# Kernel tuning notes

Hardware: AMD Instinct MI355X
Metric: run time of the kernel (lower is better)

The kernel has to match this reference:

```python
import jax, jax.numpy as jnp
import numpy as np
from jax import lax

# NPZD biogeochemistry constants (fixed buffers in the torch module)
XI = 0.067; ZETA = 0.0095; LAM = 0.06; PSI = 1.46; MU = 0.25; ETA = 1.5; KAP = 1.0
DT = 0.125        # time step in days (trange[1]-trange[0])
SPD = 8           # steps per day = round(1/DT)


def weno3z(qm, q0, qp):
    eps = 1e-14
    qi1 = -0.5 * qm + 1.5 * q0
    qi2 = 0.5 * (q0 + qp)
    b1 = (q0 - qm) ** 2
    b2 = (qp - q0) ** 2
    tau = jnp.abs(b2 - b1)
    w1 = (1.0 / 3.0) * (1.0 + tau / (b1 + eps))
    w2 = (2.0 / 3.0) * (1.0 + tau / (b2 + eps))
    return (w1 * qi1 + w2 * qi2) / (w1 + w2)


def bio_step(NO3, NH4, P, Z, D, It, alpha, Xi, rho, gamma, Gamma, varphi):
    a = alpha[:, None, None]; Xi3 = Xi[:, None, None]; rho3 = rho[:, None, None]
    g3 = gamma[:, None, None]; G3 = Gamma[:, None, None]; v3 = varphi[:, None, None]
    G = ETA * a * It / jnp.sqrt(ETA ** 2 + (a * It) ** 2)
    fNO3 = NO3 / (KAP + NO3)
    fNH4 = NH4 / (KAP + NH4)
    ePsi = jnp.exp(-PSI * NH4)
    graz = rho3 * (1.0 - jnp.exp(-LAM * P)) * Z
    bNO3 = MU * NH4 - G * ePsi * P * fNO3
    bNH4 = v3 * D + G3 * Z - G * P * fNH4 - MU * NH4
    bP = G * P * (ePsi * fNO3 + fNH4) - graz - Xi3 * P
    bZ = (1.0 - g3) * graz - G3 * Z
    bD = g3 * graz + Xi3 * P - v3 * D
    return bNO3, bNH4, bP, bZ, bD


def thomas(a_inf, diag, a_sup, rhs):
    # Batched Thomas tridiagonal solve; a_inf/a_sup: [..., Nz-1], diag: [..., Nz], rhs: [..., Nz, K]
    a = jnp.moveaxis(a_inf, -1, 0)   # [Nz-1, ...]
    b = jnp.moveaxis(diag, -1, 0)    # [Nz, ...]
    c = jnp.moveaxis(a_sup, -1, 0)   # [Nz-1, ...]
    d = jnp.moveaxis(rhs, -2, 0)     # [Nz, ..., K]
    cp0 = c[0] / b[0]
    dp0 = d[0] / b[0][..., None]
    c_pad = jnp.concatenate([c[1:], jnp.zeros_like(c[:1])], axis=0)

    def fwd(carry, x):
        cp_prev, dp_prev = carry
        a_i, b_i, c_i, d_i = x
        m = b_i - a_i * cp_prev
        cp = c_i / m
        dp = (d_i - a_i[..., None] * dp_prev) / m[..., None]
        return (cp, dp), (cp, dp)

    _, (cps, dps) = lax.scan(fwd, (cp0, dp0), (a, b[1:], c_pad, d[1:]))
    cps = jnp.concatenate([cp0[None], cps], axis=0)
    dps = jnp.concatenate([dp0[None], dps], axis=0)

    def bwd(x_next, x):
        cp_i, dp_i = x
        x_i = dp_i - cp_i[..., None] * x_next
        return x_i, x_i

    xN = dps[-1]
    _, x_rest = lax.scan(bwd, xN, (cps[:-1], dps[:-1]), reverse=True)
    x = jnp.concatenate([x_rest, xN[None]], axis=0)
    return jnp.moveaxis(x, 0, -2)


def sed_flux(T, sedc, dzT, dzw):
    # Sedimentation flux at interfaces, weno3z interior, upwind boundaries
    Ns, nw, Nz = T.shape
    inner = sedc * weno3z(T[:, :, :-2] * dzT[:-2], T[:, :, 1:-1] * dzT[1:-1], T[:, :, 2:] * dzT[2:]) / dzw[2:-1]
    flux = jnp.zeros((Ns, nw, Nz + 1), T.dtype)
    flux = flux.at[:, :, 2:-1].set(inner)
    flux = flux.at[:, :, 1:2].set(sedc * T[:, :, :1])
    flux = flux.at[:, :, -1:].set(sedc * T[:, :, -1:])
    return flux


def _forward(Kz, I0, alpha, Xi, rho, gamma, Gamma, varphi, omega, beta,
             NO3_0, NH4_0, P_0, Z_0, D_0, sub_windows, zT, zw):
    Ns, nw, Nz = NO3_0.shape
    lw = sub_windows.shape[1]
    dzT = zw[1:] - zw[:-1]                                              # [Nz]
    dzw = jnp.concatenate([dzT[:1] / 2, zT[1:] - zT[:-1], dzT[-1:] / 2])  # [Nz+1]
    sw0 = sub_windows[:, 0].astype(jnp.int32)                           # [nw]
    idx2 = 2 * sw0[:, None] + jnp.arange(2 * lw)[None, :]               # half-day forcing slice
    Kz_win = Kz[:, idx2, :]                                             # [Ns, nw, 2*lw, Nz+1]
    idx1 = sw0[:, None] + jnp.arange(lw)[None, :]
    I0_win = I0[:, idx1]                                                # [Ns, nw, lw]
    r = jax.nn.relu
    rw = jnp.zeros_like(sub_windows)
    for t in range(1):  # round(trange[-1]/365) == 1 year of forcing
        rw = rw + (1.0 / 20.0) * (r(sub_windows - (30 + 365 * t)) - r(sub_windows - (31 + 365 * t))
                                  - r(sub_windows - (60 + 365 * t)) + r(sub_windows - (61 + 365 * t)))
    sedc = omega[:, None, None]
    beta3 = beta[:, None, None]
    total = (lw - 1) * SPD
    k = jnp.arange(total)
    day = k // SPD             # I0 index (day resolution)
    h2 = k // (SPD // 2)       # Kz index (half-day resolution)
    so = day + 1               # outer sub-window step being advanced to

    def step(carry, x):
        NO3, NH4, P, Z, D = carry
        d, h, s = x
        I0d = jnp.take(I0_win, d, axis=2)                               # [Ns, nw]
        It = I0d[:, :, None] * jnp.exp(-XI * zT - ZETA * jnp.cumsum(P * dzT, axis=2))
        bN, bA, bP, bZ, bD = bio_step(NO3, NH4, P, Z, D, It, alpha, Xi, rho, gamma, Gamma, varphi)
        Kzh = jnp.take(Kz_win, h, axis=2)[:, :, 1:Nz]                   # [Ns, nw, Nz-1]
        a_sup = -DT * Kzh / (dzT[:Nz - 1] * dzw[1:Nz])
        a_inf = -DT * Kzh / (dzT[1:Nz] * dzw[1:Nz])
        diag = jnp.concatenate([1 - a_sup[..., :1],
                                1 - a_inf[..., :Nz - 2] - a_sup[..., 1:Nz - 1],
                                1 - a_inf[..., Nz - 2:]], axis=-1)
        rhs = jnp.stack([NO3 + DT * bN, NH4 + DT * bA, P + DT * bP, Z + DT * bZ, D + DT * bD], axis=-1)
        sol = thomas(a_inf, diag, a_sup, rhs)                           # implicit diffusion, [Ns,nw,Nz,5]
        dN = sol[..., 0]; dA = sol[..., 1]; dP = sol[..., 2]; dZ = sol[..., 3]; dD = sol[..., 4]
        flux = sed_flux(dD, sedc, dzT, dzw)
        sD = dD + DT * (flux[:, :, :-1] - flux[:, :, 1:]) / dzT
        rap = jnp.take(rw, s, axis=1)                                   # [nw]
        nN = dN + (beta3 - dN) * rap[None, :, None]                     # nitrate nudging
        new = (nN, dA, dP, dZ, sD)
        return new, jnp.stack(new)

    carry0 = (NO3_0, NH4_0, P_0, Z_0, D_0)
    _, ys = lax.scan(step, carry0, (day, h2, so))
    frames = jnp.concatenate([jnp.stack(carry0)[None], ys[SPD - 1::SPD]], axis=0)  # [lw,5,Ns,nw,Nz]
    return jnp.transpose(frames, (2, 3, 0, 1, 4))  # [Ns, nw, lw, 5, Nz]


def setup_inputs() -> dict:
    key = jax.random.key(0)
    ks = jax.random.split(key, 16)
    Ns, nw, lw, Nz = 64, 12, 6, 200
    zw = jnp.linspace(0.0, 200.0, Nz + 1, dtype=jnp.float32)
    zT = 0.5 * (zw[:-1] + zw[1:])
    sub_windows = jnp.arange(nw * lw, dtype=jnp.float32).reshape(nw, lw)
    u = lambda k, shp, lo, hi: jax.random.uniform(k, shp, jnp.float32, lo, hi)
    inp = {
        'Kz': u(ks[0], (Ns, 2 * nw * lw + 2, Nz + 1), 0.1, 5.0),
        'I0': u(ks[1], (Ns, nw * lw + 1), 50.0, 300.0),
        'alpha': u(ks[2], (Ns,), 0.01, 0.04),
        'Xi': u(ks[3], (Ns,), 0.05, 0.15),
        'rho': u(ks[4], (Ns,), 1.0, 2.0),
        'gamma': u(ks[5], (Ns,), 0.2, 0.4),
        'Gamma': u(ks[6], (Ns,), 0.05, 0.15),
        'varphi': u(ks[7], (Ns,), 0.05, 0.15),
        'omega': u(ks[8], (Ns,), 1.0, 5.0),
        'beta': u(ks[9], (Ns,), 4.0, 8.0),
        'NO3_0': u(ks[10], (Ns, nw, Nz), 0.5, 3.0),
        'NH4_0': u(ks[11], (Ns, nw, Nz), 0.1, 1.0),
        'P_0': u(ks[12], (Ns, nw, Nz), 0.2, 1.5),
        'Z_0': u(ks[13], (Ns, nw, Nz), 0.1, 1.0),
        'D_0': u(ks[14], (Ns, nw, Nz), 0.1, 1.0),
        'sub_windows': sub_windows,
        'zT': zT,
        'zw': zw,
    }
    return inp


def reference(Kz, I0, alpha, Xi, rho, gamma, Gamma, varphi, omega, beta,
              NO3_0, NH4_0, P_0, Z_0, D_0, sub_windows, zT, zw):
    return _forward(Kz, I0, alpha, Xi, rho, gamma, Gamma, varphi, omega, beta,
                    NO3_0, NH4_0, P_0, Z_0, D_0, sub_windows, zT, zw)
```

## Files before the change

kernel.cpp:

```cpp
#include <hip/hip_runtime.h>

#define NSC 64
#define NWN 12
#define LWN 6
#define NZD 200
#define NFRAMES 6
#define NL 4
#define ACTL 50

__device__ __forceinline__ float frcp(float x) { return __builtin_amdgcn_rcpf(x); }
__device__ __forceinline__ float frsq(float x) { return __builtin_amdgcn_rsqf(x); }
#if __has_builtin(__builtin_amdgcn_exp2f)
__device__ __forceinline__ float fexp2(float x) { return __builtin_amdgcn_exp2f(x); }
#else
__device__ __forceinline__ float fexp2(float x) { return exp2f(x); }
#endif

template<int CTRL>
__device__ __forceinline__ float dppmov(float x) {
    return __int_as_float(__builtin_amdgcn_update_dpp(0, __float_as_int(x), CTRL, 0xf, 0xf, true));
}
__device__ __forceinline__ float nbr_p1(float x) { return dppmov<0x130>(x); }
__device__ __forceinline__ float nbr_m1(float x) { return dppmov<0x138>(x); }
__device__ __forceinline__ float nbr_p2(float x) { return nbr_p1(nbr_p1(x)); }
__device__ __forceinline__ float nbr_m2(float x) { return nbr_m1(nbr_m1(x)); }

template<int CTRL, int RMASK, bool BC>
__device__ __forceinline__ float dppadd(float x) {
    const int t = __builtin_amdgcn_update_dpp(0, __float_as_int(x), CTRL, RMASK, 0xf, BC);
    return x + __int_as_float(t);
}
__device__ __forceinline__ float wave_iscan(float x) {
    x = dppadd<0x111, 0xf, true>(x);
    x = dppadd<0x112, 0xf, true>(x);
    x = dppadd<0x114, 0xf, true>(x);
    x = dppadd<0x118, 0xf, true>(x);
    x = dppadd<0x142, 0xa, false>(x);
    x = dppadd<0x143, 0xc, false>(x);
    return x;
}

__device__ __forceinline__ float weno3z_b(float qm, float q0, float qp, float b1, float b2) {
    const float qi1 = 1.5f * q0 - 0.5f * qm;
    const float qi2 = 0.5f * (q0 + qp);
    const float b1e = b1 + 1e-14f;
    const float b2e = b2 + 1e-14f;
    const float tau = fabsf(b2 - b1);
    const float W1 = (b1e + tau) * b2e;
    const float W2 = 2.f * (b2e + tau) * b1e;
    return (W1 * qi1 + W2 * qi2) * frcp(W1 + W2);
}

__global__ __launch_bounds__(64, 1) void nnpzd_wave(
    const float* __restrict__ Kz, const float* __restrict__ I0,
    const float* __restrict__ alpha_p, const float* __restrict__ Xi_p,
    const float* __restrict__ rho_p, const float* __restrict__ gamma_p,
    const float* __restrict__ Gamma_p, const float* __restrict__ varphi_p,
    const float* __restrict__ omega_p, const float* __restrict__ beta_p,
    const float* __restrict__ NO3_0, const float* __restrict__ NH4_0,
    const float* __restrict__ P_0, const float* __restrict__ Z_0,
    const float* __restrict__ D_0, const float* __restrict__ subw,
    const float* __restrict__ zT, const float* __restrict__ zw,
    float* __restrict__ out)
{
    const float XI = 0.067f, ZETA = 0.0095f, LAM = 0.06f, PSI = 1.46f;
    const float MU = 0.25f, ETA = 1.5f, KAP = 1.0f, DT = 0.125f;
    const float LOG2E = 1.44269504088896340736f;
    const float ZL2 = -ZETA * LOG2E;
    const float PL2 = -PSI * LOG2E;
    const float LL2 = -LAM * LOG2E;

    const int col  = blockIdx.x;
    const int si   = col / NWN;
    const int wi   = col - si * NWN;
    const int lane = threadIdx.x;
    const bool act = lane < ACTL;
    const int  c0  = lane * NL;

    const float pa   = alpha_p[si];
    const float pXi  = Xi_p[si];
    const float prho = rho_p[si];
    const float pgam = gamma_p[si];
    const float pGam = Gamma_p[si];
    const float pvar = varphi_p[si];
    const float sedc = omega_p[si];
    const float pbet = beta_p[si];
    const int   sw0  = (int)subw[wi * LWN];

    float dzT[NL], DTdz[NL], ezT[NL], kAf[NL], kCf[NL], swN[NL], swN4;
    {
        float dzw_[NL + 2];
        #pragma unroll
        for (int j = 0; j <= NL + 1; ++j) {
            const int i = act ? (c0 + j) : 0;
            dzw_[j] = (i == 0)   ? 0.5f * (zw[1] - zw[0])
                    : (i >= NZD) ? 0.5f * (zw[NZD] - zw[NZD - 1])
                                 : (zT[i] - zT[i - 1]);
        }
        #pragma unroll
        for (int j = 0; j < NL; ++j) {
            const int i = act ? (c0 + j) : 0;
            const float dz = zw[i + 1] - zw[i];
            dzT[j]  = dz;
            DTdz[j] = act ? (DT / dz) : 0.f;
            ezT[j]  = expf(-XI * zT[i]);
            kAf[j]  = (act && (c0 + j) >= 1)       ? (-DT / (dz * dzw_[j]))     : 0.f;
            kCf[j]  = (act && (c0 + j) <= NZD - 2) ? (-DT / (dz * dzw_[j + 1])) : 0.f;
            swN[j]  = act ? (sedc / dzw_[j]) : 0.f;
        }
        swN4 = act ? (sedc / dzw_[NL]) : 0.f;
    }

    float vN[NL], vA[NL], vP[NL], vZ[NL], vD[NL];
    {
        const size_t ib = (size_t)col * NZD + c0;
        if (act) {
            const float4 n4 = *reinterpret_cast<const float4*>(&NO3_0[ib]);
            const float4 a4 = *reinterpret_cast<const float4*>(&NH4_0[ib]);
            const float4 p4 = *reinterpret_cast<const float4*>(&P_0[ib]);
            const float4 z4 = *reinterpret_cast<const float4*>(&Z_0[ib]);
            const float4 d4 = *reinterpret_cast<const float4*>(&D_0[ib]);
            vN[0]=n4.x; vN[1]=n4.y; vN[2]=n4.z; vN[3]=n4.w;
            vA[0]=a4.x; vA[1]=a4.y; vA[2]=a4.z; vA[3]=a4.w;
            vP[0]=p4.x; vP[1]=p4.y; vP[2]=p4.z; vP[3]=p4.w;
            vZ[0]=z4.x; vZ[1]=z4.y; vZ[2]=z4.z; vZ[3]=z4.w;
            vD[0]=d4.x; vD[1]=d4.y; vD[2]=d4.z; vD[3]=d4.w;
        } else {
            #pragma unroll
            for (int j = 0; j < NL; ++j) { vN[j]=vA[j]=vP[j]=vZ[j]=vD[j]=0.f; }
        }
    }

    const size_t obase = (size_t)col * (NFRAMES * 5 * NZD);
    if (act) {
        *reinterpret_cast<float4*>(&out[obase + 0 * NZD + c0]) = make_float4(vN[0],vN[1],vN[2],vN[3]);
        *reinterpret_cast<float4*>(&out[obase + 1 * NZD + c0]) = make_float4(vA[0],vA[1],vA[2],vA[3]);
        *reinterpret_cast<float4*>(&out[obase + 2 * NZD + c0]) = make_float4(vP[0],vP[1],vP[2],vP[3]);
        *reinterpret_cast<float4*>(&out[obase + 3 * NZD + c0]) = make_float4(vZ[0],vZ[1],vZ[2],vZ[3]);
        *reinterpret_cast<float4*>(&out[obase + 4 * NZD + c0]) = make_float4(vD[0],vD[1],vD[2],vD[3]);
    }

    const float* KzBase = Kz + (size_t)si * (2 * NWN * LWN + 2) * (NZD + 1);
    const float* I0row  = I0 + (size_t)si * (NWN * LWN + 1);

    float t00, t10, t11, t20, t21, t22, t30, t31, t32, t33;
    float ecf0, ecf1, ecf2;
    float aa0, aa1, aa2, cl0, cl1, cl2, cl3;
    float E1a, E2a, E1b, E2b, invbF;
    float Iez[NL];

    float kzc[NL + 1];
    {
        const float* kzp = KzBase + (size_t)(2 * sw0) * (NZD + 1);
        #pragma unroll
        for (int j = 0; j <= NL; ++j) kzc[j] = act ? kzp[c0 + j] : 0.f;
    }
    float curI0 = I0row[sw0];
    float curSw = subw[wi * LWN + 1];
    float nxtI0 = 0.f, nxtSw = 0.f;

    auto solve = [&](const float* d, float* Xo) {
        const float Ec  = ecf0 * d[0] + ecf1 * d[1] + ecf2 * d[2];
        const float En  = nbr_p1(Ec);
        const float Dt3 = t30 * d[0] + t31 * d[1] + t32 * d[2] + t33 * d[3];
        float dR = Dt3 - cl3 * En;
        dR += E1a * nbr_m1(dR) + E2a * nbr_p1(dR);
        dR += E1b * nbr_m2(dR) + E2b * nbr_p2(dR);
        const float y  = dR * invbF;
        const float xm = nbr_m1(y);
        const float Dt0 = t00 * d[0];
        const float Dt1 = t10 * d[0] + t11 * d[1];
        const float Dt2 = t20 * d[0] + t21 * d[1] + t22 * d[2];
        Xo[3] = y;
        Xo[2] = Dt2 - aa2 * xm - cl2 * Xo[3];
        Xo[1] = Dt1 - aa1 * xm - cl1 * Xo[2];
        Xo[0] = Dt0 - aa0 * xm - cl0 * Xo[1];
    };

    for (int d8 = 0; d8 < 5; ++d8) {
        if (d8 < 4) {
            nxtI0 = I0row[sw0 + d8 + 1];
            nxtSw = subw[wi * LWN + d8 + 2];
        }
        #pragma unroll
        for (int j = 0; j < NL; ++j) Iez[j] = curI0 * ezT[j];
        const float rap = 0.05f * (fminf(fmaxf(curSw - 30.f, 0.f), 1.f)
                                 - fminf(fmaxf(curSw - 60.f, 0.f), 1.f));

        for (int k4 = 0; k4 < 2; ++k4) {
            float ac_[NL], cc_[NL];
            #pragma unroll
            for (int j = 0; j < NL; ++j) {
                ac_[j] = kAf[j] * kzc[j];
                cc_[j] = kCf[j] * kzc[j + 1];
            }
            {
                const float* kzp = KzBase + (size_t)(2 * sw0 + 2 * d8 + k4 + 1) * (NZD + 1);
                #pragma unroll
                for (int j = 0; j <= NL; ++j) kzc[j] = act ? kzp[c0 + j] : 0.f;
            }
            const float iv0 = frcp(1.f - ac_[0] - cc_[0]);
            cl0 = cc_[0] * iv0;
            aa0 = ac_[0] * iv0;
            t00 = iv0;
            const float iv1 = frcp(1.f - ac_[1] - cc_[1] - ac_[1] * cl0);
            const float qf1 = ac_[1] * iv1;
            cl1 = cc_[1] * iv1;
            aa1 = -qf1 * aa0;
            t11 = iv1; t10 = -qf1 * t00;
            const float iv2 = frcp(1.f - ac_[2] - cc_[2] - ac_[2] * cl1);
            const float qf2 = ac_[2] * iv2;
            cl2 = cc_[2] * iv2;
            aa2 = -qf2 * aa1;
            t22 = iv2; t21 = -qf2 * t11; t20 = -qf2 * t10;
            const float iv3 = frcp(1.f - ac_[3] - cc_[3] - ac_[3] * cl2);
            const float qf3 = ac_[3] * iv3;
            cl3 = cc_[3] * iv3;
            const float aa3 = -qf3 * aa2;
            t33 = iv3; t32 = -qf3 * t22; t31 = -qf3 * t21; t30 = -qf3 * t20;
            const float c01 = cl0 * cl1;
            ecf0 = t00 - cl0 * t10 + c01 * t20;
            ecf1 = -cl0 * t11 + c01 * t21;
            ecf2 = c01 * t22;
            const float F = aa0 - cl0 * (aa1 - cl1 * aa2);
            const float G = cl0 * cl1 * cl2;
            const float Fn = nbr_p1(F);
            const float Gn = nbr_p1(G);
            float aR = aa3;
            float bR = 1.f - cl3 * Fn;
            float cR = -cl3 * Gn;
            if (!act) { aR = 0.f; bR = 1.f; cR = 0.f; }
            const float ib  = frcp(bR);
            const float am  = nbr_m1(aR), ibm = nbr_m1(ib), cm = nbr_m1(cR);
            const float ap  = nbr_p1(aR), ibp = nbr_p1(ib), cp = nbr_p1(cR);
            E1a = -aR * ibm;
            E2a = -cR * ibp;
            const float b1r = bR + E1a * cm + E2a * ap;
            const float a1r = E1a * am;
            const float c1r = E2a * cp;
            const float ib1  = frcp(b1r);
            const float am2  = nbr_m2(a1r), ib1m = nbr_m2(ib1), cm2 = nbr_m2(c1r);
            const float ap2  = nbr_p2(a1r), ib1p = nbr_p2(ib1), cp2 = nbr_p2(c1r);
            E1b = -a1r * ib1m;
            E2b = -c1r * ib1p;
            invbF = frcp(b1r + E1b * cm2 + E2b * ap2);

            #pragma unroll
            for (int k2 = 0; k2 < 4; ++k2) {
                float cl_[NL];
                float run = 0.f;
                #pragma unroll
                for (int j = 0; j < NL; ++j) { run += vP[j] * dzT[j]; cl_[j] = run; }
                const float pref = wave_iscan(run) - run;

                float grz[NL], ddZ[NL], ddD[NL];
                #pragma unroll
                for (int j = 0; j < NL; ++j) {
                    grz[j] = prho * (1.f - fexp2(LL2 * vP[j])) * vZ[j];
                    ddZ[j] = vZ[j] + DT * ((1.f - pgam) * grz[j] - pGam * vZ[j]);
                    ddD[j] = vD[j] + DT * (pgam * grz[j] + pXi * vP[j] - pvar * vD[j]);
                }
                float XD[NL];
                solve(ddD, XD);

                float dd0[NL], dd1[NL], dd2[NL];
                #pragma unroll
                for (int j = 0; j < NL; ++j) {
                    const float It  = Iez[j] * fexp2(ZL2 * (pref + cl_[j]));
                    const float aIt = pa * It;
                    const float Gg  = ETA * aIt * frsq(ETA * ETA + aIt * aIt);
                    const float dN  = KAP + vN[j];
                    const float dA  = KAP + vA[j];
                    const float ir  = frcp(dN * dA);
                    const float fN  = vN[j] * dA * ir;
                    const float fA  = vA[j] * dN * ir;
                    const float eP  = fexp2(PL2 * vA[j]);
                    const float GP  = Gg * vP[j];
                    const float bN = MU * vA[j] - GP * eP * fN;
                    const float bA = pvar * vD[j] + pGam * vZ[j] - GP * fA - MU * vA[j];
                    const float bP = GP * (eP * fN + fA) - grz[j] - pXi * vP[j];
                    dd0[j] = vN[j] + DT * bN;
                    dd1[j] = vA[j] + DT * bA;
                    dd2[j] = vP[j] + DT * bP;
                }

                float q[NL];
                #pragma unroll
                for (int j = 0; j < NL; ++j) q[j] = XD[j] * dzT[j];
                const float qm1 = nbr_m1(q[3]);
                const float qm2 = nbr_m1(q[2]);
                const float dq0 = q[0] - qm1;
                const float dq1 = q[1] - q[0];
                const float dq2 = q[2] - q[1];
                const float dq3 = q[3] - q[2];
                const float s0 = dq0 * dq0, s1 = dq1 * dq1, s2 = dq2 * dq2, s3 = dq3 * dq3;
                const float s4 = nbr_p1(s0);
                const float sm = nbr_m1(s3);
                const float qn0 = q[3] + nbr_p1(dq0);
                const float f0 = (lane == 0) ? 0.f           : weno3z_b(qm2, qm1, q[0], sm, s0) * swN[0];
                const float f1 = (lane == 0) ? sedc * XD[0]  : weno3z_b(qm1, q[0], q[1], s0, s1) * swN[1];
                const float f2 = weno3z_b(q[0], q[1], q[2], s1, s2) * swN[2];
                const float f3 = weno3z_b(q[1], q[2], q[3], s2, s3) * swN[3];
                const float f4 = (lane == ACTL - 1) ? sedc * XD[3]
                                                    : weno3z_b(q[2], q[3], qn0, s3, s4) * swN4;
                const float fs[NL + 1] = { f0, f1, f2, f3, f4 };
                #pragma unroll
                for (int j = 0; j < NL; ++j)
                    vD[j] = XD[j] + (fs[j] - fs[j + 1]) * DTdz[j];

                float XZ[NL], X0[NL], X1[NL], X2[NL];
                solve(ddZ, XZ);
                solve(dd0, X0);
                solve(dd1, X1);
                solve(dd2, X2);
                #pragma unroll
                for (int j = 0; j < NL; ++j) {
                    vZ[j] = XZ[j];
                    vN[j] = X0[j] + (pbet - X0[j]) * rap;
                    vA[j] = X1[j];
                    vP[j] = X2[j];
                }

                if (k4 == 1 && k2 == 3 && act) {
                    const size_t ob = obase + (size_t)(d8 + 1) * (5 * NZD) + c0;
                    *reinterpret_cast<float4*>(&out[ob + 0 * NZD]) = make_float4(vN[0],vN[1],vN[2],vN[3]);
                    *reinterpret_cast<float4*>(&out[ob + 1 * NZD]) = make_float4(vA[0],vA[1],vA[2],vA[3]);
                    *reinterpret_cast<float4*>(&out[ob + 2 * NZD]) = make_float4(vP[0],vP[1],vP[2],vP[3]);
                    *reinterpret_cast<float4*>(&out[ob + 3 * NZD]) = make_float4(vZ[0],vZ[1],vZ[2],vZ[3]);
                    *reinterpret_cast<float4*>(&out[ob + 4 * NZD]) = make_float4(vD[0],vD[1],vD[2],vD[3]);
                }
            }
        }
        if (d8 < 4) { curI0 = nxtI0; curSw = nxtSw; }
    }
}

extern "C" void kernel_launch(void* const* d_in, const int* in_sizes, int n_in,
                              void* d_out, int out_size, void* d_ws, size_t ws_size,
                              hipStream_t stream) {
    const float* Kz    = (const float*)d_in[0];
    const float* I0    = (const float*)d_in[1];
    const float* alpha = (const float*)d_in[2];
    const float* Xi    = (const float*)d_in[3];
    const float* rho   = (const float*)d_in[4];
    const float* gam   = (const float*)d_in[5];
    const float* Gam   = (const float*)d_in[6];
    const float* varp  = (const float*)d_in[7];
    const float* omg   = (const float*)d_in[8];
    const float* bet   = (const float*)d_in[9];
    const float* N0    = (const float*)d_in[10];
    const float* A0    = (const float*)d_in[11];
    const float* P0    = (const float*)d_in[12];
    const float* Z0    = (const float*)d_in[13];
    const float* Dd0   = (const float*)d_in[14];
    const float* sbw   = (const float*)d_in[15];
    const float* zTp   = (const float*)d_in[16];
    const float* zwp   = (const float*)d_in[17];
    float* out = (float*)d_out;

    dim3 grid(NSC * NWN);
    dim3 block(64);
    hipLaunchKernelGGL(nnpzd_wave, grid, block, 0, stream,
                       Kz, I0, alpha, Xi, rho, gam, Gam, varp, omg, bet,
                       N0, A0, P0, Z0, Dd0, sbw, zTp, zwp, out);
}
```

Before: 56.77 us.

## Reorder solves to overlap light scan, use bpermute for distance-2 exchanges

The phytoplankton tridiagonal solve now runs first, so the light-attenuation prefix scan for the next step is computed right after it and overlaps with the remaining solves, instead of sitting at the start of each step. The second reduction stage folds the inverse pivot into precomputed coefficients, which removes one sequential dependency, and uses ds_bpermute for the two-lane shifts instead of two chained DPP moves. The bpermute calls go through LDS hardware and add latency, and initialising the scan before the loop changes where that work sits.

```diff
diff --git a/kernel.cpp b/kernel.cpp
--- a/kernel.cpp
+++ b/kernel.cpp
@@ -15,6 +15,9 @@
 #else
 __device__ __forceinline__ float fexp2(float x) { return exp2f(x); }
 #endif
+__device__ __forceinline__ float bperm(int addr, float v) {
+    return __int_as_float(__builtin_amdgcn_ds_bpermute(addr, __float_as_int(v)));
+}
 
 template<int CTRL>
 __device__ __forceinline__ float dppmov(float x) {
@@ -77,6 +80,10 @@
     const bool act = lane < ACTL;
     const int  c0  = lane * NL;
 
+    const int aM1 = ((lane > 0) ? lane - 1 : 0) * 4;
+    const int aU2 = ((lane >= 2) ? lane - 2 : 0) * 4;
+    const int aD2 = ((lane + 2 < 64) ? lane + 2 : 63) * 4;
+
     const float pa   = alpha_p[si];
     const float pXi  = Xi_p[si];
     const float prho = rho_p[si];
@@ -146,7 +153,7 @@
     float t00, t10, t11, t20, t21, t22, t30, t31, t32, t33;
     float ecf0, ecf1, ecf2;
     float aa0, aa1, aa2, cl0, cl1, cl2, cl3;
-    float E1a, E2a, E1b, E2b, invbF;
+    float E1a, E2a, ivF, E1bF, E2bF;
     float Iez[NL];
 
     float kzc[NL + 1];
@@ -158,6 +165,14 @@
     float curI0 = I0row[sw0];
     float curSw = subw[wi * LWN + 1];
     float nxtI0 = 0.f, nxtSw = 0.f;
+
+    float clC[NL], prefC;
+    {
+        float run = 0.f;
+        #pragma unroll
+        for (int j = 0; j < NL; ++j) { run += vP[j] * dzT[j]; clC[j] = run; }
+        prefC = wave_iscan(run) - run;
+    }
 
     auto solve = [&](const float* d, float* Xo) {
         const float Ec  = ecf0 * d[0] + ecf1 * d[1] + ecf2 * d[2];
@@ -165,9 +180,10 @@
         const float Dt3 = t30 * d[0] + t31 * d[1] + t32 * d[2] + t33 * d[3];
         float dR = Dt3 - cl3 * En;
         dR += E1a * nbr_m1(dR) + E2a * nbr_p1(dR);
-        dR += E1b * nbr_m2(dR) + E2b * nbr_p2(dR);
-        const float y  = dR * invbF;
-        const float xm = nbr_m1(y);
+        const float dm2 = bperm(aU2, dR);
+        const float dp2 = bperm(aD2, dR);
+        const float y   = ivF * dR + E1bF * dm2 + E2bF * dp2;
+        const float xm  = bperm(aM1, y);
         const float Dt0 = t00 * d[0];
         const float Dt1 = t10 * d[0] + t11 * d[1];
         const float Dt2 = t20 * d[0] + t21 * d[1] + t22 * d[2];
@@ -241,18 +257,15 @@
             const float ib1  = frcp(b1r);
             const float am2  = nbr_m2(a1r), ib1m = nbr_m2(ib1), cm2 = nbr_m2(c1r);
             const float ap2  = nbr_p2(a1r), ib1p = nbr_p2(ib1), cp2 = nbr_p2(c1r);
-            E1b = -a1r * ib1m;
-            E2b = -c1r * ib1p;
-            invbF = frcp(b1r + E1b * cm2 + E2b * ap2);
+            const float E1b = -a1r * ib1m;
+            const float E2b = -c1r * ib1p;
+            const float invbF = frcp(b1r + E1b * cm2 + E2b * ap2);
+            ivF  = invbF;
+            E1bF = E1b * invbF;
+            E2bF = E2b * invbF;
 
             #pragma unroll
             for (int k2 = 0; k2 < 4; ++k2) {
-                float cl_[NL];
-                float run = 0.f;
-                #pragma unroll
-                for (int j = 0; j < NL; ++j) { run += vP[j] * dzT[j]; cl_[j] = run; }
-                const float pref = wave_iscan(run) - run;
-
                 float grz[NL], ddZ[NL], ddD[NL];
                 #pragma unroll
                 for (int j = 0; j < NL; ++j) {
@@ -260,13 +273,11 @@
                     ddZ[j] = vZ[j] + DT * ((1.f - pgam) * grz[j] - pGam * vZ[j]);
                     ddD[j] = vD[j] + DT * (pgam * grz[j] + pXi * vP[j] - pvar * vD[j]);
                 }
-                float XD[NL];
-                solve(ddD, XD);
 
                 float dd0[NL], dd1[NL], dd2[NL];
                 #pragma unroll
                 for (int j = 0; j < NL; ++j) {
-                    const float It  = Iez[j] * fexp2(ZL2 * (pref + cl_[j]));
+                    const float It  = Iez[j] * fexp2(ZL2 * (prefC + clC[j]));
                     const float aIt = pa * It;
                     const float Gg  = ETA * aIt * frsq(ETA * ETA + aIt * aIt);
                     const float dN  = KAP + vN[j];
@@ -283,6 +294,19 @@
                     dd1[j] = vA[j] + DT * bA;
                     dd2[j] = vP[j] + DT * bP;
                 }
+
+                float XP[NL], XD[NL];
+                solve(dd2, XP);
+                #pragma unroll
+                for (int j = 0; j < NL; ++j) vP[j] = XP[j];
+                {
+                    float run = 0.f;
+                    #pragma unroll
+                    for (int j = 0; j < NL; ++j) { run += vP[j] * dzT[j]; clC[j] = run; }
+                    prefC = wave_iscan(run) - run;
+                }
+
+                solve(ddD, XD);
 
                 float q[NL];
                 #pragma unroll
@@ -308,17 +332,15 @@
                 for (int j = 0; j < NL; ++j)
                     vD[j] = XD[j] + (fs[j] - fs[j + 1]) * DTdz[j];
 
-                float XZ[NL], X0[NL], X1[NL], X2[NL];
+                float XZ[NL], X0[NL], X1[NL];
                 solve(ddZ, XZ);
                 solve(dd0, X0);
                 solve(dd1, X1);
-                solve(dd2, X2);
                 #pragma unroll
                 for (int j = 0; j < NL; ++j) {
                     vZ[j] = XZ[j];
                     vN[j] = X0[j] + (pbet - X0[j]) * rap;
                     vA[j] = X1[j];
-                    vP[j] = X2[j];
                 }
 
                 if (k4 == 1 && k2 == 3 && act) {
```

New measurement: 58.92 us. 3.8% more time.

## Process two water columns per wave using packed float2 arithmetic

Applied to the files above, without the earlier changes.

Each 64-lane block now integrates two adjacent columns at once, storing every state and solver coefficient as a two-wide float vector so arithmetic can map to packed FP32 instructions. The grid is halved to match. The intent is to raise instruction-level parallelism and hide the latency of the serial DPP scans and transcendental ops. In exchange, register pressure roughly doubles and fewer blocks are available to spread across CUs.

```diff
diff --git a/kernel.cpp b/kernel.cpp
--- a/kernel.cpp
+++ b/kernel.cpp
@@ -8,6 +8,8 @@
 #define NL 4
 #define ACTL 50
 
+typedef float v2f __attribute__((ext_vector_type(2)));
+
 __device__ __forceinline__ float frcp(float x) { return __builtin_amdgcn_rcpf(x); }
 __device__ __forceinline__ float frsq(float x) { return __builtin_amdgcn_rsqf(x); }
 #if __has_builtin(__builtin_amdgcn_exp2f)
@@ -16,14 +18,23 @@
 __device__ __forceinline__ float fexp2(float x) { return exp2f(x); }
 #endif
 
+__device__ __forceinline__ v2f v2s(float s)            { v2f r; r.x = s;  r.y = s;  return r; }
+__device__ __forceinline__ v2f v2mk(float a, float b)  { v2f r; r.x = a;  r.y = b;  return r; }
+__device__ __forceinline__ v2f v2rcp(v2f x)  { return v2mk(frcp(x.x),  frcp(x.y)); }
+__device__ __forceinline__ v2f v2rsq(v2f x)  { return v2mk(frsq(x.x),  frsq(x.y)); }
+__device__ __forceinline__ v2f v2exp2(v2f x) { return v2mk(fexp2(x.x), fexp2(x.y)); }
+__device__ __forceinline__ v2f v2abs(v2f x)  { return v2mk(fabsf(x.x), fabsf(x.y)); }
+
 template<int CTRL>
 __device__ __forceinline__ float dppmov(float x) {
     return __int_as_float(__builtin_amdgcn_update_dpp(0, __float_as_int(x), CTRL, 0xf, 0xf, true));
 }
-__device__ __forceinline__ float nbr_p1(float x) { return dppmov<0x130>(x); }
-__device__ __forceinline__ float nbr_m1(float x) { return dppmov<0x138>(x); }
-__device__ __forceinline__ float nbr_p2(float x) { return nbr_p1(nbr_p1(x)); }
-__device__ __forceinline__ float nbr_m2(float x) { return nbr_m1(nbr_m1(x)); }
+template<int CTRL>
+__device__ __forceinline__ v2f dppmov2(v2f x) { return v2mk(dppmov<CTRL>(x.x), dppmov<CTRL>(x.y)); }
+__device__ __forceinline__ v2f nbr_p1(v2f x) { return dppmov2<0x130>(x); }
+__device__ __forceinline__ v2f nbr_m1(v2f x) { return dppmov2<0x138>(x); }
+__device__ __forceinline__ v2f nbr_p2(v2f x) { return nbr_p1(nbr_p1(x)); }
+__device__ __forceinline__ v2f nbr_m2(v2f x) { return nbr_m1(nbr_m1(x)); }
 
 template<int CTRL, int RMASK, bool BC>
 __device__ __forceinline__ float dppadd(float x) {
@@ -39,16 +50,17 @@
     x = dppadd<0x143, 0xc, false>(x);
     return x;
 }
-
-__device__ __forceinline__ float weno3z_b(float qm, float q0, float qp, float b1, float b2) {
-    const float qi1 = 1.5f * q0 - 0.5f * qm;
-    const float qi2 = 0.5f * (q0 + qp);
-    const float b1e = b1 + 1e-14f;
-    const float b2e = b2 + 1e-14f;
-    const float tau = fabsf(b2 - b1);
-    const float W1 = (b1e + tau) * b2e;
-    const float W2 = 2.f * (b2e + tau) * b1e;
-    return (W1 * qi1 + W2 * qi2) * frcp(W1 + W2);
+__device__ __forceinline__ v2f wave_iscan2(v2f x) { return v2mk(wave_iscan(x.x), wave_iscan(x.y)); }
+
+__device__ __forceinline__ v2f weno3z_v(v2f qm, v2f q0, v2f qp, v2f b1, v2f b2) {
+    const v2f qi1 = 1.5f * q0 - 0.5f * qm;
+    const v2f qi2 = 0.5f * (q0 + qp);
+    const v2f b1e = b1 + 1e-14f;
+    const v2f b2e = b2 + 1e-14f;
+    const v2f tau = v2abs(b2 - b1);
+    const v2f W1 = (b1e + tau) * b2e;
+    const v2f W2 = 2.f * (b2e + tau) * b1e;
+    return (W1 * qi1 + W2 * qi2) * v2rcp(W1 + W2);
 }
 
 __global__ __launch_bounds__(64, 1) void nnpzd_wave(
@@ -70,9 +82,9 @@
     const float PL2 = -PSI * LOG2E;
     const float LL2 = -LAM * LOG2E;
 
-    const int col  = blockIdx.x;
-    const int si   = col / NWN;
-    const int wi   = col - si * NWN;
+    const int col0 = blockIdx.x * 2;
+    const int si   = col0 / NWN;
+    const int wi0  = col0 - si * NWN;
     const int lane = threadIdx.x;
     const bool act = lane < ACTL;
     const int  c0  = lane * NL;
@@ -85,7 +97,8 @@
     const float pvar = varphi_p[si];
     const float sedc = omega_p[si];
     const float pbet = beta_p[si];
-    const int   sw0  = (int)subw[wi * LWN];
+    const int sw0a = (int)subw[wi0 * LWN];
+    const int sw0b = (int)subw[(wi0 + 1) * LWN];
 
     float dzT[NL], DTdz[NL], ezT[NL], kAf[NL], kCf[NL], swN[NL], swN4;
     {
@@ -111,66 +124,77 @@
         swN4 = act ? (sedc / dzw_[NL]) : 0.f;
     }
 
-    float vN[NL], vA[NL], vP[NL], vZ[NL], vD[NL];
+    v2f vN[NL], vA[NL], vP[NL], vZ[NL], vD[NL];
     {
-        const size_t ib = (size_t)col * NZD + c0;
+        const size_t ib0 = (size_t)col0 * NZD + c0;
+        const size_t ib1 = ib0 + NZD;
         if (act) {
-            const float4 n4 = *reinterpret_cast<const float4*>(&NO3_0[ib]);
-            const float4 a4 = *reinterpret_cast<const float4*>(&NH4_0[ib]);
-            const float4 p4 = *reinterpret_cast<const float4*>(&P_0[ib]);
-            const float4 z4 = *reinterpret_cast<const float4*>(&Z_0[ib]);
-            const float4 d4 = *reinterpret_cast<const float4*>(&D_0[ib]);
-            vN[0]=n4.x; vN[1]=n4.y; vN[2]=n4.z; vN[3]=n4.w;
-            vA[0]=a4.x; vA[1]=a4.y; vA[2]=a4.z; vA[3]=a4.w;
-            vP[0]=p4.x; vP[1]=p4.y; vP[2]=p4.z; vP[3]=p4.w;
-            vZ[0]=z4.x; vZ[1]=z4.y; vZ[2]=z4.z; vZ[3]=z4.w;
-            vD[0]=d4.x; vD[1]=d4.y; vD[2]=d4.z; vD[3]=d4.w;
+            const float4 nx = *reinterpret_cast<const float4*>(&NO3_0[ib0]);
+            const float4 ny = *reinterpret_cast<const float4*>(&NO3_0[ib1]);
+            const float4 ax = *reinterpret_cast<const float4*>(&NH4_0[ib0]);
+            const float4 ay = *reinterpret_cast<const float4*>(&NH4_0[ib1]);
+            const float4 px = *reinterpret_cast<const float4*>(&P_0[ib0]);
+            const float4 py = *reinterpret_cast<const float4*>(&P_0[ib1]);
+            const float4 zx = *reinterpret_cast<const float4*>(&Z_0[ib0]);
+            const float4 zy = *reinterpret_cast<const float4*>(&Z_0[ib1]);
+            const float4 dx = *reinterpret_cast<const float4*>(&D_0[ib0]);
+            const float4 dy = *reinterpret_cast<const float4*>(&D_0[ib1]);
+            vN[0]=v2mk(nx.x,ny.x); vN[1]=v2mk(nx.y,ny.y); vN[2]=v2mk(nx.z,ny.z); vN[3]=v2mk(nx.w,ny.w);
+            vA[0]=v2mk(ax.x,ay.x); vA[1]=v2mk(ax.y,ay.y); vA[2]=v2mk(ax.z,ay.z); vA[3]=v2mk(ax.w,ay.w);
+            vP[0]=v2mk(px.x,py.x); vP[1]=v2mk(px.y,py.y); vP[2]=v2mk(px.z,py.z); vP[3]=v2mk(px.w,py.w);
+            vZ[0]=v2mk(zx.x,zy.x); vZ[1]=v2mk(zx.y,zy.y); vZ[2]=v2mk(zx.z,zy.z); vZ[3]=v2mk(zx.w,zy.w);
+            vD[0]=v2mk(dx.x,dy.x); vD[1]=v2mk(dx.y,dy.y); vD[2]=v2mk(dx.z,dy.z); vD[3]=v2mk(dx.w,dy.w);
         } else {
             #pragma unroll
-            for (int j = 0; j < NL; ++j) { vN[j]=vA[j]=vP[j]=vZ[j]=vD[j]=0.f; }
-        }
-    }
-
-    const size_t obase = (size_t)col * (NFRAMES * 5 * NZD);
+            for (int j = 0; j < NL; ++j) { vN[j]=vA[j]=vP[j]=vZ[j]=vD[j]=v2s(0.f); }
+        }
+    }
+
+    const size_t ob0base = (size_t)col0 * (NFRAMES * 5 * NZD);
+    const size_t ob1base = ob0base + (size_t)(NFRAMES * 5 * NZD);
     if (act) {
-        *reinterpret_cast<float4*>(&out[obase + 0 * NZD + c0]) = make_float4(vN[0],vN[1],vN[2],vN[3]);
-        *reinterpret_cast<float4*>(&out[obase + 1 * NZD + c0]) = make_float4(vA[0],vA[1],vA[2],vA[3]);
-        *reinterpret_cast<float4*>(&out[obase + 2 * NZD + c0]) = make_float4(vP[0],vP[1],vP[2],vP[3]);
-        *reinterpret_cast<float4*>(&out[obase + 3 * NZD + c0]) = make_float4(vZ[0],vZ[1],vZ[2],vZ[3]);
-        *reinterpret_cast<float4*>(&out[obase + 4 * NZD + c0]) = make_float4(vD[0],vD[1],vD[2],vD[3]);
+        #define WRFRAME(base, comp)                                                                   \
+            *reinterpret_cast<float4*>(&out[(base) + 0 * NZD + c0]) = make_float4(vN[0].comp,vN[1].comp,vN[2].comp,vN[3].comp); \
+            *reinterpret_cast<float4*>(&out[(base) + 1 * NZD + c0]) = make_float4(vA[0].comp,vA[1].comp,vA[2].comp,vA[3].comp); \
+            *reinterpret_cast<float4*>(&out[(base) + 2 * NZD + c0]) = make_float4(vP[0].comp,vP[1].comp,vP[2].comp,vP[3].comp); \
+            *reinterpret_cast<float4*>(&out[(base) + 3 * NZD + c0]) = make_float4(vZ[0].comp,vZ[1].comp,vZ[2].comp,vZ[3].comp); \
+            *reinterpret_cast<float4*>(&out[(base) + 4 * NZD + c0]) = make_float4(vD[0].comp,vD[1].comp,vD[2].comp,vD[3].comp);
+        WRFRAME(ob0base, x)
+        WRFRAME(ob1base, y)
     }
 
     const float* KzBase = Kz + (size_t)si * (2 * NWN * LWN + 2) * (NZD + 1);
     const float* I0row  = I0 + (size_t)si * (NWN * LWN + 1);
 
-    float t00, t10, t11, t20, t21, t22, t30, t31, t32, t33;
-    float ecf0, ecf1, ecf2;
-    float aa0, aa1, aa2, cl0, cl1, cl2, cl3;
-    float E1a, E2a, E1b, E2b, invbF;
-    float Iez[NL];
-
-    float kzc[NL + 1];
+    v2f t00, t10, t11, t20, t21, t22, t30, t31, t32, t33;
+    v2f ecf0, ecf1, ecf2;
+    v2f aa0, aa1, aa2, cl0, cl1, cl2, cl3;
+    v2f E1a, E2a, E1b, E2b, invbF;
+    v2f Iez[NL];
+
+    v2f kzc[NL + 1];
     {
-        const float* kzp = KzBase + (size_t)(2 * sw0) * (NZD + 1);
+        const float* k0 = KzBase + (size_t)(2 * sw0a) * (NZD + 1);
+        const float* k1 = KzBase + (size_t)(2 * sw0b) * (NZD + 1);
         #pragma unroll
-        for (int j = 0; j <= NL; ++j) kzc[j] = act ? kzp[c0 + j] : 0.f;
-    }
-    float curI0 = I0row[sw0];
-    float curSw = subw[wi * LWN + 1];
-    float nxtI0 = 0.f, nxtSw = 0.f;
-
-    auto solve = [&](const float* d, float* Xo) {
-        const float Ec  = ecf0 * d[0] + ecf1 * d[1] + ecf2 * d[2];
-        const float En  = nbr_p1(Ec);
-        const float Dt3 = t30 * d[0] + t31 * d[1] + t32 * d[2] + t33 * d[3];
-        float dR = Dt3 - cl3 * En;
+        for (int j = 0; j <= NL; ++j) kzc[j] = act ? v2mk(k0[c0 + j], k1[c0 + j]) : v2s(0.f);
+    }
+    v2f curI0 = v2mk(I0row[sw0a], I0row[sw0b]);
+    v2f curSw = v2mk(subw[wi0 * LWN + 1], subw[(wi0 + 1) * LWN + 1]);
+    v2f nxtI0 = v2s(0.f), nxtSw = v2s(0.f);
+
+    auto solve = [&](const v2f* d, v2f* Xo) {
+        const v2f Ec  = ecf0 * d[0] + ecf1 * d[1] + ecf2 * d[2];
+        const v2f En  = nbr_p1(Ec);
+        const v2f Dt3 = t30 * d[0] + t31 * d[1] + t32 * d[2] + t33 * d[3];
+        v2f dR = Dt3 - cl3 * En;
         dR += E1a * nbr_m1(dR) + E2a * nbr_p1(dR);
         dR += E1b * nbr_m2(dR) + E2b * nbr_p2(dR);
-        const float y  = dR * invbF;
-        const float xm = nbr_m1(y);
-        const float Dt0 = t00 * d[0];
-        const float Dt1 = t10 * d[0] + t11 * d[1];
-        const float Dt2 = t20 * d[0] + t21 * d[1] + t22 * d[2];
+        const v2f y  = dR * invbF;
+        const v2f xm = nbr_m1(y);
+        const v2f Dt0 = t00 * d[0];
+        const v2f Dt1 = t10 * d[0] + t11 * d[1];
+        const v2f Dt2 = t20 * d[0] + t21 * d[1] + t22 * d[2];
         Xo[3] = y;
         Xo[2] = Dt2 - aa2 * xm - cl2 * Xo[3];
         Xo[1] = Dt1 - aa1 * xm - cl1 * Xo[2];
@@ -179,136 +203,139 @@
 
     for (int d8 = 0; d8 < 5; ++d8) {
         if (d8 < 4) {
-            nxtI0 = I0row[sw0 + d8 + 1];
-            nxtSw = subw[wi * LWN + d8 + 2];
+            nxtI0 = v2mk(I0row[sw0a + d8 + 1], I0row[sw0b + d8 + 1]);
+            nxtSw = v2mk(subw[wi0 * LWN + d8 + 2], subw[(wi0 + 1) * LWN + d8 + 2]);
         }
         #pragma unroll
         for (int j = 0; j < NL; ++j) Iez[j] = curI0 * ezT[j];
-        const float rap = 0.05f * (fminf(fmaxf(curSw - 30.f, 0.f), 1.f)
-                                 - fminf(fmaxf(curSw - 60.f, 0.f), 1.f));
+        v2f rap;
+        rap.x = 0.05f * (fminf(fmaxf(curSw.x - 30.f, 0.f), 1.f) - fminf(fmaxf(curSw.x - 60.f, 0.f), 1.f));
+        rap.y = 0.05f * (fminf(fmaxf(curSw.y - 30.f, 0.f), 1.f) - fminf(fmaxf(curSw.y - 60.f, 0.f), 1.f));
 
         for (int k4 = 0; k4 < 2; ++k4) {
-            float ac_[NL], cc_[NL];
+            v2f ac_[NL], cc_[NL];
             #pragma unroll
             for (int j = 0; j < NL; ++j) {
                 ac_[j] = kAf[j] * kzc[j];
                 cc_[j] = kCf[j] * kzc[j + 1];
             }
             {
-                const float* kzp = KzBase + (size_t)(2 * sw0 + 2 * d8 + k4 + 1) * (NZD + 1);
-                #pragma unroll
-                for (int j = 0; j <= NL; ++j) kzc[j] = act ? kzp[c0 + j] : 0.f;
+                const int r = 2 * d8 + k4 + 1;
+                const float* k0 = KzBase + (size_t)(2 * sw0a + r) * (NZD + 1);
+                const float* k1 = KzBase + (size_t)(2 * sw0b + r) * (NZD + 1);
+                #pragma unroll
+                for (int j = 0; j <= NL; ++j) kzc[j] = act ? v2mk(k0[c0 + j], k1[c0 + j]) : v2s(0.f);
             }
-            const float iv0 = frcp(1.f - ac_[0] - cc_[0]);
+            const v2f iv0 = v2rcp(1.f - ac_[0] - cc_[0]);
             cl0 = cc_[0] * iv0;
             aa0 = ac_[0] * iv0;
             t00 = iv0;
-            const float iv1 = frcp(1.f - ac_[1] - cc_[1] - ac_[1] * cl0);
-            const float qf1 = ac_[1] * iv1;
+            const v2f iv1 = v2rcp(1.f - ac_[1] - cc_[1] - ac_[1] * cl0);
+            const v2f qf1 = ac_[1] * iv1;
             cl1 = cc_[1] * iv1;
             aa1 = -qf1 * aa0;
             t11 = iv1; t10 = -qf1 * t00;
-            const float iv2 = frcp(1.f - ac_[2] - cc_[2] - ac_[2] * cl1);
-            const float qf2 = ac_[2] * iv2;
+            const v2f iv2 = v2rcp(1.f - ac_[2] - cc_[2] - ac_[2] * cl1);
+            const v2f qf2 = ac_[2] * iv2;
             cl2 = cc_[2] * iv2;
             aa2 = -qf2 * aa1;
             t22 = iv2; t21 = -qf2 * t11; t20 = -qf2 * t10;
-            const float iv3 = frcp(1.f - ac_[3] - cc_[3] - ac_[3] * cl2);
-            const float qf3 = ac_[3] * iv3;
+            const v2f iv3 = v2rcp(1.f - ac_[3] - cc_[3] - ac_[3] * cl2);
+            const v2f qf3 = ac_[3] * iv3;
             cl3 = cc_[3] * iv3;
-            const float aa3 = -qf3 * aa2;
+            const v2f aa3 = -qf3 * aa2;
             t33 = iv3; t32 = -qf3 * t22; t31 = -qf3 * t21; t30 = -qf3 * t20;
-            const float c01 = cl0 * cl1;
+            const v2f c01 = cl0 * cl1;
             ecf0 = t00 - cl0 * t10 + c01 * t20;
             ecf1 = -cl0 * t11 + c01 * t21;
             ecf2 = c01 * t22;
-            const float F = aa0 - cl0 * (aa1 - cl1 * aa2);
-            const float G = cl0 * cl1 * cl2;
-            const float Fn = nbr_p1(F);
-            const float Gn = nbr_p1(G);
-            float aR = aa3;
-            float bR = 1.f - cl3 * Fn;
-            float cR = -cl3 * Gn;
-            if (!act) { aR = 0.f; bR = 1.f; cR = 0.f; }
-            const float ib  = frcp(bR);
-            const float am  = nbr_m1(aR), ibm = nbr_m1(ib), cm = nbr_m1(cR);
-            const float ap  = nbr_p1(aR), ibp = nbr_p1(ib), cp = nbr_p1(cR);
+            const v2f F = aa0 - cl0 * (aa1 - cl1 * aa2);
+            const v2f G = cl0 * cl1 * cl2;
+            const v2f Fn = nbr_p1(F);
+            const v2f Gn = nbr_p1(G);
+            v2f aR = aa3;
+            v2f bR = 1.f - cl3 * Fn;
+            v2f cR = -cl3 * Gn;
+            if (!act) { aR = v2s(0.f); bR = v2s(1.f); cR = v2s(0.f); }
+            const v2f ib  = v2rcp(bR);
+            const v2f am  = nbr_m1(aR), ibm = nbr_m1(ib), cm = nbr_m1(cR);
+            const v2f ap  = nbr_p1(aR), ibp = nbr_p1(ib), cp = nbr_p1(cR);
             E1a = -aR * ibm;
             E2a = -cR * ibp;
-            const float b1r = bR + E1a * cm + E2a * ap;
-            const float a1r = E1a * am;
-            const float c1r = E2a * cp;
-            const float ib1  = frcp(b1r);
-            const float am2  = nbr_m2(a1r), ib1m = nbr_m2(ib1), cm2 = nbr_m2(c1r);
-            const float ap2  = nbr_p2(a1r), ib1p = nbr_p2(ib1), cp2 = nbr_p2(c1r);
+            const v2f b1r = bR + E1a * cm + E2a * ap;
+            const v2f a1r = E1a * am;
+            const v2f c1r = E2a * cp;
+            const v2f ib1  = v2rcp(b1r);
+            const v2f am2  = nbr_m2(a1r), ib1m = nbr_m2(ib1), cm2 = nbr_m2(c1r);
+            const v2f ap2  = nbr_p2(a1r), ib1p = nbr_p2(ib1), cp2 = nbr_p2(c1r);
             E1b = -a1r * ib1m;
             E2b = -c1r * ib1p;
-            invbF = frcp(b1r + E1b * cm2 + E2b * ap2);
+            invbF = v2rcp(b1r + E1b * cm2 + E2b * ap2);
 
             #pragma unroll
             for (int k2 = 0; k2 < 4; ++k2) {
-                float cl_[NL];
-                float run = 0.f;
+                v2f cl_[NL];
+                v2f run = v2s(0.f);
                 #pragma unroll
                 for (int j = 0; j < NL; ++j) { run += vP[j] * dzT[j]; cl_[j] = run; }
-                const float pref = wave_iscan(run) - run;
-
-                float grz[NL], ddZ[NL], ddD[NL];
+                const v2f pref = wave_iscan2(run) - run;
+
+                v2f grz[NL], ddZ[NL], ddD[NL];
                 #pragma unroll
                 for (int j = 0; j < NL; ++j) {
-                    grz[j] = prho * (1.f - fexp2(LL2 * vP[j])) * vZ[j];
+                    grz[j] = prho * (1.f - v2exp2(LL2 * vP[j])) * vZ[j];
                     ddZ[j] = vZ[j] + DT * ((1.f - pgam) * grz[j] - pGam * vZ[j]);
                     ddD[j] = vD[j] + DT * (pgam * grz[j] + pXi * vP[j] - pvar * vD[j]);
                 }
-                float XD[NL];
+                v2f XD[NL];
                 solve(ddD, XD);
 
-                float dd0[NL], dd1[NL], dd2[NL];
+                v2f dd0[NL], dd1[NL], dd2[NL];
                 #pragma unroll
                 for (int j = 0; j < NL; ++j) {
-                    const float It  = Iez[j] * fexp2(ZL2 * (pref + cl_[j]));
-                    const float aIt = pa * It;
-                    const float Gg  = ETA * aIt * frsq(ETA * ETA + aIt * aIt);
-                    const float dN  = KAP + vN[j];
-                    const float dA  = KAP + vA[j];
-                    const float ir  = frcp(dN * dA);
-                    const float fN  = vN[j] * dA * ir;
-                    const float fA  = vA[j] * dN * ir;
-                    const float eP  = fexp2(PL2 * vA[j]);
-                    const float GP  = Gg * vP[j];
-                    const float bN = MU * vA[j] - GP * eP * fN;
-                    const float bA = pvar * vD[j] + pGam * vZ[j] - GP * fA - MU * vA[j];
-                    const float bP = GP * (eP * fN + fA) - grz[j] - pXi * vP[j];
+                    const v2f It  = Iez[j] * v2exp2(ZL2 * (pref + cl_[j]));
+                    const v2f aIt = pa * It;
+                    const v2f Gg  = ETA * aIt * v2rsq(ETA * ETA + aIt * aIt);
+                    const v2f dN  = KAP + vN[j];
+                    const v2f dA  = KAP + vA[j];
+                    const v2f ir  = v2rcp(dN * dA);
+                    const v2f fN  = vN[j] * dA * ir;
+                    const v2f fA  = vA[j] * dN * ir;
+                    const v2f eP  = v2exp2(PL2 * vA[j]);
+                    const v2f GP  = Gg * vP[j];
+                    const v2f bN = MU * vA[j] - GP * eP * fN;
+                    const v2f bA = pvar * vD[j] + pGam * vZ[j] - GP * fA - MU * vA[j];
+                    const v2f bP = GP * (eP * fN + fA) - grz[j] - pXi * vP[j];
                     dd0[j] = vN[j] + DT * bN;
                     dd1[j] = vA[j] + DT * bA;
                     dd2[j] = vP[j] + DT * bP;
                 }
 
-                float q[NL];
+                v2f q[NL];
                 #pragma unroll
                 for (int j = 0; j < NL; ++j) q[j] = XD[j] * dzT[j];
-                const float qm1 = nbr_m1(q[3]);
-                const float qm2 = nbr_m1(q[2]);
-                const float dq0 = q[0] - qm1;
-                const float dq1 = q[1] - q[0];
-                const float dq2 = q[2] - q[1];
-                const float dq3 = q[3] - q[2];
-                const float s0 = dq0 * dq0, s1 = dq1 * dq1, s2 = dq2 * dq2, s3 = dq3 * dq3;
-                const float s4 = nbr_p1(s0);
-                const float sm = nbr_m1(s3);
-                const float qn0 = q[3] + nbr_p1(dq0);
-                const float f0 = (lane == 0) ? 0.f           : weno3z_b(qm2, qm1, q[0], sm, s0) * swN[0];
-                const float f1 = (lane == 0) ? sedc * XD[0]  : weno3z_b(qm1, q[0], q[1], s0, s1) * swN[1];
-                const float f2 = weno3z_b(q[0], q[1], q[2], s1, s2) * swN[2];
-                const float f3 = weno3z_b(q[1], q[2], q[3], s2, s3) * swN[3];
-                const float f4 = (lane == ACTL - 1) ? sedc * XD[3]
-                                                    : weno3z_b(q[2], q[3], qn0, s3, s4) * swN4;
-                const float fs[NL + 1] = { f0, f1, f2, f3, f4 };
+                const v2f qm1 = nbr_m1(q[3]);
+                const v2f qm2 = nbr_m1(q[2]);
+                const v2f dq0 = q[0] - qm1;
+                const v2f dq1 = q[1] - q[0];
+                const v2f dq2 = q[2] - q[1];
+                const v2f dq3 = q[3] - q[2];
+                const v2f s0 = dq0 * dq0, s1 = dq1 * dq1, s2 = dq2 * dq2, s3 = dq3 * dq3;
+                const v2f s4 = nbr_p1(s0);
+                const v2f sm = nbr_m1(s3);
+                const v2f qn0 = q[3] + nbr_p1(dq0);
+                const v2f f0 = (lane == 0) ? v2s(0.f)    : weno3z_v(qm2, qm1, q[0], sm, s0) * swN[0];
+                const v2f f1 = (lane == 0) ? sedc * XD[0] : weno3z_v(qm1, q[0], q[1], s0, s1) * swN[1];
+                const v2f f2 = weno3z_v(q[0], q[1], q[2], s1, s2) * swN[2];
+                const v2f f3 = weno3z_v(q[1], q[2], q[3], s2, s3) * swN[3];
+                const v2f f4 = (lane == ACTL - 1) ? sedc * XD[3]
+                                                  : weno3z_v(q[2], q[3], qn0, s3, s4) * swN4;
+                const v2f fs[NL + 1] = { f0, f1, f2, f3, f4 };
                 #pragma unroll
                 for (int j = 0; j < NL; ++j)
                     vD[j] = XD[j] + (fs[j] - fs[j + 1]) * DTdz[j];
 
-                float XZ[NL], X0[NL], X1[NL], X2[NL];
+                v2f XZ[NL], X0[NL], X1[NL], X2[NL];
                 solve(ddZ, XZ);
                 solve(dd0, X0);
                 solve(dd1, X1);
@@ -322,17 +349,17 @@
                 }
 
                 if (k4 == 1 && k2 == 3 && act) {
-                    const size_t ob = obase + (size_t)(d8 + 1) * (5 * NZD) + c0;
-                    *reinterpret_cast<float4*>(&out[ob + 0 * NZD]) = make_float4(vN[0],vN[1],vN[2],vN[3]);
-                    *reinterpret_cast<float4*>(&out[ob + 1 * NZD]) = make_float4(vA[0],vA[1],vA[2],vA[3]);
-                    *reinterpret_cast<float4*>(&out[ob + 2 * NZD]) = make_float4(vP[0],vP[1],vP[2],vP[3]);
-                    *reinterpret_cast<float4*>(&out[ob + 3 * NZD]) = make_float4(vZ[0],vZ[1],vZ[2],vZ[3]);
-                    *reinterpret_cast<float4*>(&out[ob + 4 * NZD]) = make_float4(vD[0],vD[1],vD[2],vD[3]);
+                    const size_t fo = (size_t)(d8 + 1) * (5 * NZD);
+                    const size_t b0 = ob0base + fo;
+                    const size_t b1 = ob1base + fo;
+                    WRFRAME(b0, x)
+                    WRFRAME(b1, y)
                 }
             }
         }
         if (d8 < 4) { curI0 = nxtI0; curSw = nxtSw; }
     }
+    #undef WRFRAME
 }
 
 extern "C" void kernel_launch(void* const* d_in, const int* in_sizes, int n_in,
@@ -358,7 +385,7 @@
     const float* zwp   = (const float*)d_in[17];
     float* out = (float*)d_out;
 
-    dim3 grid(NSC * NWN);
+    dim3 grid(NSC * NWN / 2);
     dim3 block(64);
     hipLaunchKernelGGL(nnpzd_wave, grid, block, 0, stream,
                        Kz, I0, alpha, Xi, rho, gam, Gam, varp, omg, bet,
```

Result: slower. 67.52 us (+18.9%).
